# Kernel tuning notes

Measured on AMD Instinct MI355X. Metric: run time of the kernel, lower is better.

## Reference

```python
import jax, jax.numpy as jnp
import numpy as np

# DNC dims: N memory slots, WM word size, R read heads, H controller hidden, D word_vec
N, WM, R, H, D = 256, 64, 4, 512, 512
T, B = 128, 32
EPS = 1e-6
IFACE = R*WM + R + WM + 1 + WM + WM + R + 1 + 1 + 3*R  # DNC interface vector size


def setup_inputs() -> dict:
    key = jax.random.key(0)
    k = jax.random.split(key, 8)
    in_dim = D + R*WM  # controller sees [x_t ; flattened read vectors]
    w = lambda kk, shape: jax.random.normal(kk, shape, jnp.float32) * 0.02
    return {
        "emb_utt": jax.random.normal(k[0], (T, B, D), jnp.float32),
        "Wx": w(k[1], (in_dim, 4*H)),
        "Wh": w(k[2], (H, 4*H)),
        "b_lstm": jnp.zeros((4*H,), jnp.float32),
        "W_pre": w(k[3], (H, D)),
        "b_pre": jnp.zeros((D,), jnp.float32),
        "W_iface": w(k[4], (H, IFACE)),
        "b_iface": jnp.zeros((IFACE,), jnp.float32),
        "W_rout": w(k[5], (R*WM, D)),
    }


def _content(M, keys, beta):
    # M: (B,N,WM); keys: (B,K,WM); beta: (B,K) -> content weighting (B,K,N)
    Mn = M / jnp.maximum(jnp.linalg.norm(M, axis=-1, keepdims=True), EPS)
    kn = keys / jnp.maximum(jnp.linalg.norm(keys, axis=-1, keepdims=True), EPS)
    sim = jnp.einsum('bkw,bnw->bkn', kn, Mn)
    return jax.nn.softmax(beta[..., None] * sim, axis=-1)


def _allocation(u):
    # usage-sort-based allocation weighting (Graves et al. 2016)
    idx = jnp.argsort(u, axis=1)  # ascending usage
    su = jnp.take_along_axis(u, idx, axis=1)
    excl = jnp.concatenate([jnp.ones_like(su[:, :1]), jnp.cumprod(su, axis=1)[:, :-1]], axis=1)
    a_sorted = (1.0 - su) * excl
    bidx = jnp.arange(u.shape[0])[:, None]
    return jnp.zeros_like(u).at[bidx, idx].set(a_sorted)


def reference(emb_utt, Wx, Wh, b_lstm, W_pre, b_pre, W_iface, b_iface, W_rout):
    Bsz = emb_utt.shape[1]
    eye = jnp.eye(N, dtype=emb_utt.dtype)

    def step(carry, x):
        h, c, M, usage, rw, ww, prec, link, rvec = carry
        # ---- controller (LSTM) ----
        xin = jnp.concatenate([x, rvec.reshape(Bsz, -1)], axis=1)
        gates = xin @ Wx + h @ Wh + b_lstm
        i, f, g, o = jnp.split(gates, 4, axis=1)
        c = jax.nn.sigmoid(f) * c + jax.nn.sigmoid(i) * jnp.tanh(g)
        h = jax.nn.sigmoid(o) * jnp.tanh(c)
        # ---- interface ----
        z = h @ W_iface + b_iface
        off = [0]
        def take(n):
            v = z[:, off[0]:off[0]+n]; off[0] += n; return v
        read_keys = take(R*WM).reshape(Bsz, R, WM)
        read_str = 1.0 + jax.nn.softplus(take(R))
        write_key = take(WM)
        write_str = 1.0 + jax.nn.softplus(take(1))
        erase = jax.nn.sigmoid(take(WM))
        write_vec = take(WM)
        free = jax.nn.sigmoid(take(R))
        alloc_g = jax.nn.sigmoid(take(1))
        write_g = jax.nn.sigmoid(take(1))
        modes = jax.nn.softmax(take(3*R).reshape(Bsz, R, 3), axis=-1)
        # ---- memory write ----
        retention = jnp.prod(1.0 - free[:, :, None] * rw, axis=1)   # (B,N)
        usage = (usage + ww - usage * ww) * retention
        alloc = _allocation(usage)
        cw = _content(M, write_key[:, None, :], write_str)[:, 0, :]  # (B,N)
        ww = write_g * (alloc_g * alloc + (1.0 - alloc_g) * cw)
        M = M * (1.0 - ww[:, :, None] * erase[:, None, :]) + ww[:, :, None] * write_vec[:, None, :]
        # temporal link matrix + precedence
        link = (1.0 - ww[:, :, None] - ww[:, None, :]) * link + ww[:, :, None] * prec[:, None, :]
        link = link * (1.0 - eye)
        prec = (1.0 - jnp.sum(ww, axis=1, keepdims=True)) * prec + ww
        # ---- memory read ----
        cr = _content(M, read_keys, read_str)                        # (B,R,N)
        fw = jnp.einsum('bij,brj->bri', link, rw)                    # forward
        bw = jnp.einsum('bji,brj->bri', link, rw)                    # backward
        rw = modes[..., 0:1] * bw + modes[..., 1:2] * cr + modes[..., 2:3] * fw
        rvec = jnp.einsum('brn,bnw->brw', rw, M)
        out = h @ W_pre + b_pre + rvec.reshape(Bsz, -1) @ W_rout
        return (h, c, M, usage, rw, ww, prec, link, rvec), out

    z = lambda *s: jnp.zeros(s, jnp.float32)
    carry0 = (z(Bsz, H), z(Bsz, H), jnp.full((Bsz, N, WM), EPS, jnp.float32),
              z(Bsz, N), z(Bsz, R, N), z(Bsz, N), z(Bsz, N),
              z(Bsz, N, N), z(Bsz, R, WM))
    _, outs = jax.lax.scan(step, carry0, emb_utt)
    return outs  # (T, B, D)
```

## Files before the change

kernel.cpp:

```cpp
#include <hip/hip_runtime.h>
#include <math.h>

#define TN   256
#define TWM  64
#define TR   4
#define TH   512
#define TD   512
#define TT   128
#define TB   32
#define IFACE 471
#define EPSI 1e-6f

#define OFF_H      0
#define OFF_C      32768
#define OFF_M      49152
#define OFF_USAGE  573440
#define OFF_RW     581632
#define OFF_WW     614400
#define OFF_PRECA  622592
#define OFF_LINK   638976
#define OFF_RVEC   2736128
#define OFF_MNORM  2744320
#define OFF_ZP     2752512
#define OFF_PARSE  2998272
#define OFF_CRS    3012608
#define OFF_FW     3045376
#define OFF_BWP    3078144
#define OFF_CNT    3340288
#define TOTAL_STATE 3341696

#define CNT_ZPG(g) (OFF_CNT + (g)*16)
#define CNT_SB(b)  (OFF_CNT + (8+(b))*16)
#define CNT_FA(b)  (OFF_CNT + (40+(b))*16)
#define CNT_GG(g)  (OFF_CNT + (72+(g))*16)

__device__ __forceinline__ float sigm(float x)  { return 1.0f / (1.0f + expf(-x)); }
__device__ __forceinline__ float softpl(float x){ return x > 20.0f ? x : log1pf(expf(x)); }

__device__ __forceinline__ float ldc(const float* p) {
    return __hip_atomic_load(p, __ATOMIC_RELAXED, __HIP_MEMORY_SCOPE_AGENT);
}
__device__ __forceinline__ void stc(float* p, float v) {
    __hip_atomic_store(p, v, __ATOMIC_RELAXED, __HIP_MEMORY_SCOPE_AGENT);
}
__device__ __forceinline__ float4 ldcv4(const float* p) {
    float4 v;
    v.x = ldc(p); v.y = ldc(p + 1); v.z = ldc(p + 2); v.w = ldc(p + 3);
    return v;
}
__device__ __forceinline__ void stcv4(float* p, float4 v) {
    stc(p, v.x); stc(p + 1, v.y); stc(p + 2, v.z); stc(p + 3, v.w);
}

__global__ void k_init(float* ws) {
    int idx = blockIdx.x * 256 + threadIdx.x;
    if (idx >= TOTAL_STATE) return;
    float v = 0.0f;
    if (idx >= OFF_M && idx < OFF_M + TB*TN*TWM) v = EPSI;
    if (idx >= OFF_MNORM && idx < OFF_MNORM + TB*TN) v = 8e-6f;
    ws[idx] = v;
}

__device__ __forceinline__ void out_phase(
    const float* __restrict__ W_pre, const float* __restrict__ b_pre,
    const float* __restrict__ W_rout, const float* __restrict__ ws,
    float* __restrict__ out, float* sm, const int tid, const int B2, const int t)
{
    float* act_s = sm;
    float* red_s = sm + 3072;
    const int q = B2 >> 5, s = (B2 >> 3) & 3, bg = B2 & 7, b0 = bg * 4;
    for (int i = tid; i < 768; i += 512) {
        const int bb = i / 192;
        const int k0 = (i - bb*192) * 4;
        const float* src = (k0 < 512) ? &ws[OFF_H + (t&1)*(TB*TH) + (b0+bb)*TH + k0]
                                      : &ws[OFF_RVEC + (b0+bb)*256 + (k0 - 512)];
        *(float4*)&act_s[bb*768 + k0] = *(const float4*)src;
    }
    __syncthreads();
    const int c0 = q*128 + s*32;
    const int col = tid & 31;
    const int ksb = tid >> 5;
    float a0=0, a1=0, a2=0, a3=0;
    for (int kk = ksb*48; kk < ksb*48 + 48; ++kk) {
        const float w = (kk < 512) ? W_pre[(size_t)kk * 512 + c0 + col]
                                   : W_rout[(size_t)(kk - 512) * 512 + c0 + col];
        a0 += act_s[kk]        * w;
        a1 += act_s[768 + kk]  * w;
        a2 += act_s[1536 + kk] * w;
        a3 += act_s[2304 + kk] * w;
    }
    red_s[(ksb*4 + 0)*32 + col] = a0;
    red_s[(ksb*4 + 1)*32 + col] = a1;
    red_s[(ksb*4 + 2)*32 + col] = a2;
    red_s[(ksb*4 + 3)*32 + col] = a3;
    __syncthreads();
    if (tid < 128) {
        const int cc = tid & 31, bb = tid >> 5;
        float ssum = 0.0f;
        #pragma unroll
        for (int ks2 = 0; ks2 < 16; ++ks2) ssum += red_s[(ks2*4 + bb)*32 + cc];
        ssum += b_pre[c0 + cc];
        out[(size_t)(t - 1) * (TB * TD) + (b0+bb) * TD + c0 + cc] = ssum;
    }
}

__device__ void stepA_fn(const float* __restrict__ b_if, float* __restrict__ ws,
                         const int t, const int b, const int tid, float* sm)
{
    float* z_s      = sm + 0;
    float* rwf_s    = sm + 480;
    float* ww_old_s = sm + 1504;
    float* ww_s     = sm + 1760;
    float* u_s      = sm + 2016;
    float* prec_s   = sm + 2272;
    float* mnorm_s  = sm + 2528;
    float* alloc_s  = sm + 2784;
    float* cw_s     = sm + 3040;
    float* keysp    = sm + 3296;
    float* wkey_s   = sm + 3552;
    float* erase_s  = sm + 3616;
    float* wvec_s   = sm + 3680;
    float* rstr_s   = sm + 3744;
    float* free_s   = sm + 3748;
    float* modesp   = sm + 3752;
    float* knorm_s  = sm + 3764;
    float* sredA_s  = sm + 3772;
    float* sc_s     = sm + 3780;
    float* Pt_s     = sm + 3788;

    const float* wsM = ws + OFF_M + b * (TN * TWM);
    const float* precOld = ws + OFF_PRECA + (t & 1) * (TB * TN) + b * 256;
    float* precNew = ws + OFF_PRECA + ((t + 1) & 1) * (TB * TN) + b * 256;

    if (tid < 256)       { *(float4*)&rwf_s[tid*4] = *(const float4*)&ws[OFF_RW + b*1024 + tid*4]; }
    else if (tid < 320)  { const int i = tid-256; *(float4*)&ww_old_s[i*4] = *(const float4*)&ws[OFF_WW + b*256 + i*4]; }
    else if (tid < 384)  { const int i = tid-320; *(float4*)&u_s[i*4]      = *(const float4*)&ws[OFF_USAGE + b*256 + i*4]; }
    else if (tid < 448)  { const int i = tid-384; *(float4*)&prec_s[i*4]   = *(const float4*)&precOld[i*4]; }
    else                 { const int i = tid-448; *(float4*)&mnorm_s[i*4]  = *(const float4*)&ws[OFF_MNORM + b*256 + i*4]; }
    if (tid < IFACE) {
        float part[16];
        #pragma unroll
        for (int p = 0; p < 16; ++p)
            part[p] = ldc(&ws[OFF_ZP + ((size_t)p*32 + b) * 480 + tid]);
        float zv = b_if[tid];
        #pragma unroll
        for (int p = 0; p < 16; ++p) zv += part[p];
        z_s[tid] = zv;
    }
    __syncthreads();

    if (tid < IFACE) {
        const float v = z_s[tid];
        if (tid < 256)       keysp[(tid >> 6)*64 + (tid & 63)] = v;
        else if (tid < 260)  rstr_s[tid - 256] = 1.0f + softpl(v);
        else if (tid < 324)  wkey_s[tid - 260] = v;
        else if (tid == 324) sc_s[0] = 1.0f + softpl(v);
        else if (tid < 389)  erase_s[tid - 325] = sigm(v);
        else if (tid < 453)  wvec_s[tid - 389] = v;
        else if (tid < 457)  free_s[tid - 453] = sigm(v);
        else if (tid == 457) sc_s[1] = sigm(v);
        else if (tid == 458) sc_s[2] = sigm(v);
    }
    __syncthreads();
    if (tid < 320) {
        const int w5 = tid >> 6, lane = tid & 63;
        const float v = (w5 == 0) ? wkey_s[lane] : keysp[(w5 - 1)*64 + lane];
        float s = v * v;
        #pragma unroll
        for (int m = 1; m <= 32; m <<= 1) s += __shfl_xor(s, m);
        if (lane == 0) knorm_s[w5] = fmaxf(sqrtf(s), EPSI);
    } else if (tid >= 508) {
        const int r = tid - 508;
        const float m0 = z_s[459 + r*3], m1 = z_s[460 + r*3], m2 = z_s[461 + r*3];
        const float mx = fmaxf(m0, fmaxf(m1, m2));
        const float e0 = expf(m0 - mx), e1 = expf(m1 - mx), e2 = expf(m2 - mx);
        const float s = e0 + e1 + e2;
        modesp[r*3+0] = e0 / s; modesp[r*3+1] = e1 / s; modesp[r*3+2] = e2 / s;
    }
    __syncthreads();

    if (tid < 404) {
        float v;
        if (tid < 256)       v = keysp[tid];
        else if (tid < 320)  v = erase_s[tid - 256];
        else if (tid < 384)  v = wvec_s[tid - 320];
        else if (tid < 388)  v = rstr_s[tid - 384];
        else if (tid < 392)  v = knorm_s[tid - 388 + 1];
        else                 v = modesp[tid - 392];
        stc(&ws[OFF_PARSE + b * 448 + tid], v);
    }
    if (tid < 256) {
        float ret = 1.0f;
        #pragma unroll
        for (int r = 0; r < 4; ++r) ret *= 1.0f - free_s[r] * rwf_s[r*256 + tid];
        const float un = (u_s[tid] + ww_old_s[tid] - u_s[tid] * ww_old_s[tid]) * ret;
        u_s[tid] = un;
        ws[OFF_USAGE + b * 256 + tid] = un;
    }
    __syncthreads();

    {
        const int q = tid >> 8, n = tid & 255;
        const float un = u_s[n];
        float p = 1.0f;
        #pragma unroll 8
        for (int m = q * 128; m < q * 128 + 128; ++m) {
            const float um = u_s[m];
            const bool lt = (um < un) || (um == un && m < n);
            p *= lt ? um : 1.0f;
        }
        Pt_s[q * 256 + n] = p;
    }
    __syncthreads();
    if (tid < 256)
        alloc_s[tid] = (1.0f - u_s[tid]) * Pt_s[tid] * Pt_s[256 + tid];
    __syncthreads();

    {
        const int n = tid >> 1, q2 = tid & 1;
        const float* mp = wsM + n * 64 + q2 * 32;
        float s = 0.0f;
        #pragma unroll
        for (int it = 0; it < 8; ++it) {
            float4 mv = *(const float4*)(mp + it * 4);
            float4 kv = *(const float4*)&wkey_s[q2 * 32 + it * 4];
            s += mv.x*kv.x + mv.y*kv.y + mv.z*kv.z + mv.w*kv.w;
        }
        s += __shfl_xor(s, 1);
        if (q2 == 0) cw_s[n] = sc_s[0] * s / (knorm_s[0] * mnorm_s[n]);
    }
    __syncthreads();
    {
        float v = 0.0f, e = 0.0f;
        if (tid < 256) {
            v = cw_s[tid];
            float m = v;
            #pragma unroll
            for (int mm = 1; mm <= 32; mm <<= 1) m = fmaxf(m, __shfl_xor(m, mm));
            if ((tid & 63) == 0) sredA_s[tid >> 6] = m;
        }
        __syncthreads();
        if (tid == 0) sc_s[4] = fmaxf(fmaxf(sredA_s[0], sredA_s[1]), fmaxf(sredA_s[2], sredA_s[3]));
        __syncthreads();
        if (tid < 256) {
            e = expf(v - sc_s[4]);
            float s2 = e;
            #pragma unroll
            for (int mm = 1; mm <= 32; mm <<= 1) s2 += __shfl_xor(s2, mm);
            if ((tid & 63) == 0) sredA_s[tid >> 6] = s2;
        }
        __syncthreads();
        if (tid == 0) sc_s[5] = sredA_s[0] + sredA_s[1] + sredA_s[2] + sredA_s[3];
        __syncthreads();
        if (tid < 256) cw_s[tid] = e / sc_s[5];
    }
    __syncthreads();

    if (tid < 256) {
        const float wwn = sc_s[2] * (sc_s[1] * alloc_s[tid] + (1.0f - sc_s[1]) * cw_s[tid]);
        ww_s[tid] = wwn;
        stc(&ws[OFF_WW + b * 256 + tid], wwn);
    }
    __syncthreads();
    if (tid < 256) {
        float s = ww_s[tid];
        #pragma unroll
        for (int mm = 1; mm <= 32; mm <<= 1) s += __shfl_xor(s, mm);
        if ((tid & 63) == 0) sredA_s[tid >> 6] = s;
    }
    __syncthreads();
    if (tid == 0) sc_s[3] = sredA_s[0] + sredA_s[1] + sredA_s[2] + sredA_s[3];
    __syncthreads();
    if (tid < 256)
        precNew[tid] = (1.0f - sc_s[3]) * prec_s[tid] + ww_s[tid];
}

__device__ void stepB_fn(float* __restrict__ ws, const int t, const int b,
                         const int tid, float* sm)
{
    float* crp     = sm;
    float* rw2_s   = sm + 1024;
    float* Lt2     = sm + 2048;
    float* md      = sm + 4096;
    float* sredA_s = sm + 4112;
    float* sredB_s = sm + 4120;
    float* gmax_s  = sm + 4128;
    float* gsum_s  = sm + 4132;
    const float* wsM = ws + OFF_M + b * (TN * TWM);

    crp[tid]       = ldc(&ws[OFF_CRS + b*1024 + tid]);
    crp[tid + 512] = ldc(&ws[OFF_CRS + b*1024 + tid + 512]);
    if (tid < 12) md[tid] = ldc(&ws[OFF_PARSE + b*448 + 392 + tid]);
    __syncthreads();

    {
        const int rr = tid >> 8, n = tid & 255, wv = tid >> 6, lane = tid & 63;
        float v0 = crp[rr*256 + n], v1 = crp[(rr + 2)*256 + n];
        float m0 = v0, m1 = v1;
        #pragma unroll
        for (int mm = 1; mm <= 32; mm <<= 1) {
            m0 = fmaxf(m0, __shfl_xor(m0, mm));
            m1 = fmaxf(m1, __shfl_xor(m1, mm));
        }
        if (lane == 0) { sredA_s[wv] = m0; sredB_s[wv] = m1; }
        __syncthreads();
        if (tid < 4) {
            const float* base = (tid & 2) ? sredB_s : sredA_s;
            const int off = (tid & 1) * 4;
            gmax_s[tid] = fmaxf(fmaxf(base[off], base[off+1]), fmaxf(base[off+2], base[off+3]));
        }
        __syncthreads();
        const float e0 = expf(v0 - gmax_s[rr]);
        const float e1 = expf(v1 - gmax_s[rr + 2]);
        float s0 = e0, s1 = e1;
        #pragma unroll
        for (int mm = 1; mm <= 32; mm <<= 1) {
            s0 += __shfl_xor(s0, mm); s1 += __shfl_xor(s1, mm);
        }
        if (lane == 0) { sredA_s[wv] = s0; sredB_s[wv] = s1; }
        __syncthreads();
        if (tid < 4) {
            const float* base = (tid & 2) ? sredB_s : sredA_s;
            const int off = (tid & 1) * 4;
            gsum_s[tid] = base[off] + base[off+1] + base[off+2] + base[off+3];
        }
        __syncthreads();
        crp[rr*256 + n]       = e0 / gsum_s[rr];
        crp[(rr + 2)*256 + n] = e1 / gsum_s[rr + 2];
    }
    __syncthreads();

    {
        const int rr = tid >> 8, n = tid & 255;
        #pragma unroll
        for (int p = 0; p < 2; ++p) {
            const int r = rr + 2 * p;
            float part[8];
            #pragma unroll
            for (int c = 0; c < 8; ++c)
                part[c] = ldc(&ws[OFF_BWP + (size_t)(b*8 + c)*1024 + r*256 + n]);
            const float fwv = ldc(&ws[OFF_FW + b*1024 + r*256 + n]);
            float bw = 0.0f;
            #pragma unroll
            for (int c = 0; c < 8; ++c) bw += part[c];
            const float v = md[r*3] * bw + md[r*3+1] * crp[r*256 + n] + md[r*3+2] * fwv;
            rw2_s[r*256 + n] = v;
            ws[OFF_RW + b*1024 + r*256 + n] = v;
        }
    }
    __syncthreads();

    {
        const int g8 = tid >> 6, w = tid & 63;
        float p0=0, p1=0, p2=0, p3=0;
        const float* mb = wsM + (size_t)(g8 * 32) * 64 + w;
        for (int gg = 0; gg < 4; ++gg) {
            float mv[8];
            #pragma unroll
            for (int j = 0; j < 8; ++j) mv[j] = ldc(mb + (gg*8 + j) * 64);
            #pragma unroll
            for (int j = 0; j < 8; ++j) {
                const int n = g8*32 + gg*8 + j;
                p0 += rw2_s[n]       * mv[j];
                p1 += rw2_s[256 + n] * mv[j];
                p2 += rw2_s[512 + n] * mv[j];
                p3 += rw2_s[768 + n] * mv[j];
            }
        }
        Lt2[(g8*4 + 0)*64 + w] = p0;
        Lt2[(g8*4 + 1)*64 + w] = p1;
        Lt2[(g8*4 + 2)*64 + w] = p2;
        Lt2[(g8*4 + 3)*64 + w] = p3;
    }
    __syncthreads();
    if (tid < 256) {
        const int r = tid >> 6, w = tid & 63;
        float s = 0.0f;
        #pragma unroll
        for (int g = 0; g < 8; ++g) s += Lt2[(g*4 + r)*64 + w];
        ws[OFF_RVEC + b * 256 + tid] = s;
    }
}

__global__ __launch_bounds__(512) void k_all(
    const float* __restrict__ emb, const float* __restrict__ Wx,
    const float* __restrict__ Wh,  const float* __restrict__ b_lstm,
    const float* __restrict__ W_pre, const float* __restrict__ b_pre,
    const float* __restrict__ W_rout,
    const float* __restrict__ W_if, const float* __restrict__ b_if,
    float* __restrict__ ws, float* __restrict__ out, int t)
{
    __shared__ __align__(16) float sm[16384];
    __shared__ int myBatch;
    __shared__ int isTail;
    const int tid = threadIdx.x;
    const int blk = blockIdx.x;

    if (blk >= 128) {
        if (t > 0) {
            const int raw2 = blk - 128;
            const int B2 = (((raw2 >> 2) & 3) << 5) | ((raw2 & 3) << 3) | (raw2 >> 4);
            out_phase(W_pre, b_pre, W_rout, ws, out, sm, tid, B2, t);
        }
    } else if (t < TT) {
        const int ublk = ((blk & 7) << 4) | (blk >> 3);
        const int u0  = ublk * 4;
        {
            const int cg  = tid & 3;
            const int bg  = (tid >> 2) & 7;
            const int ks  = tid >> 5;
            const int col0 = cg * 512 + u0;
            const float* hbuf = ws + OFF_H + (t & 1) * (TB * TH);

            float acc[4][4] = {};

            for (int tile = 0; tile < 5; ++tile) {
                const int T0 = tile * 256;
                {
                    const int b = tid & 31, kf4 = tid >> 5;
                    #pragma unroll
                    for (int i = 0; i < 4; ++i) {
                        const int kf = kf4 * 4 + i;
                        const int kl = kf * 4;
                        const int k  = T0 + kl;
                        const float* src;
                        if (k < 512)      src = emb + (size_t)t * (TB*TD) + b * TD + k;
                        else if (k < 768) src = ws + OFF_RVEC + b * 256 + (k - 512);
                        else              src = hbuf + b * TH + (k - 768);
                        float4 v = *(const float4*)src;
                        sm[(kl+0)*32 + b] = v.x;
                        sm[(kl+1)*32 + b] = v.y;
                        sm[(kl+2)*32 + b] = v.z;
                        sm[(kl+3)*32 + b] = v.w;
                    }
                }
                __syncthreads();
                {
                    const int k0 = T0 + ks * 16;
                    const float* wp = (k0 < 768 ? Wx + (size_t)k0 * 2048
                                                : Wh + (size_t)(k0 - 768) * 2048) + col0;
                    const float* ap = &sm[(ks * 16) * 32 + bg * 4];
                    #pragma unroll 8
                    for (int kk = 0; kk < 16; ++kk) {
                        float4 wv = *(const float4*)wp; wp += 2048;
                        float4 av = *(const float4*)ap; ap += 32;
                        acc[0][0] += wv.x*av.x; acc[0][1] += wv.x*av.y; acc[0][2] += wv.x*av.z; acc[0][3] += wv.x*av.w;
                        acc[1][0] += wv.y*av.x; acc[1][1] += wv.y*av.y; acc[1][2] += wv.y*av.z; acc[1][3] += wv.y*av.w;
                        acc[2][0] += wv.z*av.x; acc[2][1] += wv.z*av.y; acc[2][2] += wv.z*av.z; acc[2][3] += wv.z*av.w;
                        acc[3][0] += wv.w*av.x; acc[3][1] += wv.w*av.y; acc[3][2] += wv.w*av.z; acc[3][3] += wv.w*av.w;
                    }
                }
                __syncthreads();
            }

            {
                const int rbase = 8192 + ks * 512 + (cg * 8 + bg) * 16;
                *(float4*)&sm[rbase + 0]  = make_float4(acc[0][0], acc[0][1], acc[0][2], acc[0][3]);
                *(float4*)&sm[rbase + 4]  = make_float4(acc[1][0], acc[1][1], acc[1][2], acc[1][3]);
                *(float4*)&sm[rbase + 8]  = make_float4(acc[2][0], acc[2][1], acc[2][2], acc[2][3]);
                *(float4*)&sm[rbase + 12] = make_float4(acc[3][0], acc[3][1], acc[3][2], acc[3][3]);
            }
            __syncthreads();
            {
                const int o = tid;
                float s = 0.0f;
                #pragma unroll
                for (int kq = 0; kq < 16; ++kq) s += sm[8192 + kq * 512 + o];
                const int ocg = o >> 7, obg = (o >> 4) & 7, odu = (o >> 2) & 3, obb = o & 3;
                s += b_lstm[ocg * 512 + u0 + odu];
                sm[(ocg * 4 + odu) * 32 + (obg * 4 + obb)] = s;
            }
            __syncthreads();
            if (tid < 128) {
                const int du = tid >> 5, b = tid & 31;
                const float ig = sm[(0  + du) * 32 + b];
                const float fg = sm[(4  + du) * 32 + b];
                const float gg = sm[(8  + du) * 32 + b];
                const float og = sm[(12 + du) * 32 + b];
                const int ci = b * TH + u0 + du;
                const float cold = ws[OFF_C + ci];
                const float cn = sigm(fg) * cold + sigm(ig) * tanhf(gg);
                const float hn = sigm(og) * tanhf(cn);
                ws[OFF_C + ci] = cn;
                stc(&ws[OFF_H + ((t + 1) & 1) * (TB * TH) + ci], hn);
            }
        }
        asm volatile("s_waitcnt vmcnt(0)" ::: "memory");
        __syncthreads();
        if (tid == 0)
            __hip_atomic_fetch_add((unsigned*)(ws + CNT_GG(ublk >> 3)), 1u,
                                   __ATOMIC_RELAXED, __HIP_MEMORY_SCOPE_AGENT);

        const int bgz = blk >> 4;
        const int q = (blk >> 2) & 3, s = blk & 3;
        const int b0 = bgz * 4;
        if (tid == 0) {
            const unsigned* gg = (const unsigned*)(ws + CNT_GG(q*4 + s));
            while (__hip_atomic_load(gg, __ATOMIC_RELAXED, __HIP_MEMORY_SCOPE_AGENT) < 8u * (unsigned)(t + 1))
                __builtin_amdgcn_s_sleep(2);
        }
        __syncthreads();
        {
            float* h1_s = sm;
            if (tid < 128) {
                const int bb = tid >> 5, kk = tid & 31;
                h1_s[bb*32 + kk] = ldc(&ws[OFF_H + ((t+1)&1)*(TB*TH) + (b0+bb)*TH + q*128 + s*32 + kk]);
            }
            __syncthreads();
            if (tid < IFACE) {
                const int col = tid;
                float a0=0, a1=0, a2=0, a3=0;
                const float* wb = W_if + (size_t)(q*128 + s*32) * IFACE + col;
                #pragma unroll 8
                for (int kk = 0; kk < 32; ++kk) {
                    const float w = *wb; wb += IFACE;
                    a0 += h1_s[kk]      * w;
                    a1 += h1_s[32+kk]   * w;
                    a2 += h1_s[64+kk]   * w;
                    a3 += h1_s[96+kk]   * w;
                }
                const size_t base = OFF_ZP + ((size_t)(q*4+s)*32 + b0) * 480 + col;
                stc(&ws[base],        a0);
                stc(&ws[base + 480],  a1);
                stc(&ws[base + 960],  a2);
                stc(&ws[base + 1440], a3);
            }
        }
        asm volatile("s_waitcnt vmcnt(0)" ::: "memory");
        __syncthreads();
        if (tid == 0) {
            unsigned* cnt = (unsigned*)(ws + CNT_ZPG(bgz));
            const unsigned old = __hip_atomic_fetch_add(cnt, 1u, __ATOMIC_RELAXED, __HIP_MEMORY_SCOPE_AGENT);
            const unsigned base = 16u * (unsigned)t;
            int mb = -1;
            if (old >= base + 12u) {
                mb = b0 + (int)(old - (base + 12u));
                while (__hip_atomic_load(cnt, __ATOMIC_RELAXED, __HIP_MEMORY_SCOPE_AGENT) < base + 16u)
                    __builtin_amdgcn_s_sleep(2);
            }
            myBatch = mb;
        }
        __syncthreads();
        if (myBatch >= 0) {
            stepA_fn(b_if, ws, t, myBatch, tid, sm);
            asm volatile("s_waitcnt vmcnt(0)" ::: "memory");
            __syncthreads();
            if (tid == 0)
                __hip_atomic_store((unsigned*)(ws + CNT_FA(myBatch)), (unsigned)(t + 1),
                                   __ATOMIC_RELAXED, __HIP_MEMORY_SCOPE_AGENT);
        }
    }

    if (t >= TT) return;

    const int b = blk >> 3;
    const int c = blk & 7;
    if (tid == 0) {
        const unsigned* fa = (const unsigned*)(ws + CNT_FA(b));
        while (__hip_atomic_load(fa, __ATOMIC_RELAXED, __HIP_MEMORY_SCOPE_AGENT) < (unsigned)(t + 1))
            __builtin_amdgcn_s_sleep(2);
    }
    __syncthreads();
    asm volatile("" ::: "memory");

    {
        float* ww_s   = sm;
        float* prec_s = sm + 256;
        float* rw_s   = sm + 512;
        float* pk_s   = sm + 1536;
        float* Lt     = sm + 2048;
        const float* precOld = ws + OFF_PRECA + (t & 1) * (TB * TN) + b * 256;

        if (tid < 64)        { *(float4*)&ww_s[tid*4] = ldcv4(&ws[OFF_WW + b*256 + tid*4]); }
        else if (tid < 128)  { const int i = tid-64;  *(float4*)&prec_s[i*4] = *(const float4*)&precOld[i*4]; }
        else if (tid < 384)  { const int i = tid-128; *(float4*)&rw_s[i*4]   = *(const float4*)&ws[OFF_RW + b*1024 + i*4]; }
        else if (tid < 496)  { const int i = tid-384; *(float4*)&pk_s[i*4]   = ldcv4(&ws[OFF_PARSE + b*448 + i*4]); }
        __syncthreads();

        {
            const int ric = tid >> 4, c4 = (tid & 15) * 4;
            const int gi  = c * 32 + ric;
            float* mp = ws + OFF_M + b * (TN*TWM) + gi * 64 + c4;
            float4 m = *(const float4*)mp;
            const float wwi = ww_s[gi];
            float4 er = *(const float4*)&pk_s[256 + c4];
            float4 wv = *(const float4*)&pk_s[320 + c4];
            m.x = m.x * (1.0f - wwi * er.x) + wwi * wv.x;
            m.y = m.y * (1.0f - wwi * er.y) + wwi * wv.y;
            m.z = m.z * (1.0f - wwi * er.z) + wwi * wv.z;
            m.w = m.w * (1.0f - wwi * er.w) + wwi * wv.w;
            stcv4(mp, m);
            float sn = m.x*m.x + m.y*m.y + m.z*m.z + m.w*m.w;
            float d0 = m.x*pk_s[c4]     + m.y*pk_s[c4+1]     + m.z*pk_s[c4+2]     + m.w*pk_s[c4+3];
            float d1 = m.x*pk_s[64+c4]  + m.y*pk_s[64+c4+1]  + m.z*pk_s[64+c4+2]  + m.w*pk_s[64+c4+3];
            float d2 = m.x*pk_s[128+c4] + m.y*pk_s[128+c4+1] + m.z*pk_s[128+c4+2] + m.w*pk_s[128+c4+3];
            float d3 = m.x*pk_s[192+c4] + m.y*pk_s[192+c4+1] + m.z*pk_s[192+c4+2] + m.w*pk_s[192+c4+3];
            #pragma unroll
            for (int mm = 1; mm <= 8; mm <<= 1) {
                sn += __shfl_xor(sn, mm);
                d0 += __shfl_xor(d0, mm); d1 += __shfl_xor(d1, mm);
                d2 += __shfl_xor(d2, mm); d3 += __shfl_xor(d3, mm);
            }
            if ((tid & 15) == 0) {
                const float mn = fmaxf(sqrtf(sn), EPSI);
                ws[OFF_MNORM + b*256 + gi] = mn;
                const float inv = 1.0f / mn;
                stc(&ws[OFF_CRS + b*1024 + 0*256 + gi], pk_s[384+0] * d0 * inv / pk_s[388+0]);
                stc(&ws[OFF_CRS + b*1024 + 1*256 + gi], pk_s[384+1] * d1 * inv / pk_s[388+1]);
                stc(&ws[OFF_CRS + b*1024 + 2*256 + gi], pk_s[384+2] * d2 * inv / pk_s[388+2]);
                stc(&ws[OFF_CRS + b*1024 + 3*256 + gi], pk_s[384+3] * d3 * inv / pk_s[388+3]);
            }
        }

        {
            const int j = tid & 255, p = tid >> 8;
            const float wwj = ww_s[j], pj = prec_s[j];
            #pragma unroll 4
            for (int it = 0; it < 16; ++it) {
                const int ric = it * 2 + p;
                const int gi  = c * 32 + ric;
                float* lp = ws + OFF_LINK + (size_t)b * (TN*TN) + (size_t)gi * 256 + j;
                const float wwi = ww_s[gi];
                float v = (1.0f - wwi - wwj) * (*lp) + wwi * pj;
                if (j == gi) v = 0.0f;
                *lp = v;
                Lt[ric * 257 + j] = v;
            }
        }
        __syncthreads();

        {
            const int ric = tid >> 4, g = tid & 15;
            const int gi = c * 32 + ric;
            float f0=0, f1=0, f2=0, f3=0;
            #pragma unroll 4
            for (int jj = 0; jj < 16; ++jj) {
                const int j = g * 16 + jj;
                const float v = Lt[ric * 257 + j];
                f0 += v * rw_s[j]; f1 += v * rw_s[256+j];
                f2 += v * rw_s[512+j]; f3 += v * rw_s[768+j];
            }
            #pragma unroll
            for (int mm = 1; mm <= 8; mm <<= 1) {
                f0 += __shfl_xor(f0, mm); f1 += __shfl_xor(f1, mm);
                f2 += __shfl_xor(f2, mm); f3 += __shfl_xor(f3, mm);
            }
            if (g == 0) {
                stc(&ws[OFF_FW + b*1024 + gi],       f0);
                stc(&ws[OFF_FW + b*1024 + 256 + gi], f1);
                stc(&ws[OFF_FW + b*1024 + 512 + gi], f2);
                stc(&ws[OFF_FW + b*1024 + 768 + gi], f3);
            }
        }

        {
            const int j = tid & 255, p = tid >> 8;
            float b0=0, b1=0, b2=0, b3=0;
            #pragma unroll 4
            for (int it = 0; it < 16; ++it) {
                const int ric = p * 16 + it;
                const int gi  = c * 32 + ric;
                const float v = Lt[ric * 257 + j];
                b0 += v * rw_s[gi]; b1 += v * rw_s[256+gi];
                b2 += v * rw_s[512+gi]; b3 += v * rw_s[768+gi];
            }
            __syncthreads();
            if (p == 1) { Lt[j] = b0; Lt[256+j] = b1; Lt[512+j] = b2; Lt[768+j] = b3; }
            __syncthreads();
            if (p == 0) {
                stc(&ws[OFF_BWP + (size_t)blk*1024 + j],       b0 + Lt[j]);
                stc(&ws[OFF_BWP + (size_t)blk*1024 + 256 + j], b1 + Lt[256+j]);
                stc(&ws[OFF_BWP + (size_t)blk*1024 + 512 + j], b2 + Lt[512+j]);
                stc(&ws[OFF_BWP + (size_t)blk*1024 + 768 + j], b3 + Lt[768+j]);
            }
        }
    }

    asm volatile("s_waitcnt vmcnt(0)" ::: "memory");
    __syncthreads();
    if (tid == 0) {
        unsigned* cnt = (unsigned*)(ws + CNT_SB(b));
        const unsigned old = __hip_atomic_fetch_add(cnt, 1u, __ATOMIC_RELAXED, __HIP_MEMORY_SCOPE_AGENT);
        isTail = (old == 8u * (unsigned)t + 7u) ? 1 : 0;
    }
    __syncthreads();
    if (!isTail) return;
    stepB_fn(ws, t, b, tid, sm);
}

extern "C" void kernel_launch(void* const* d_in, const int* in_sizes, int n_in,
                              void* d_out, int out_size, void* d_ws, size_t ws_size,
                              hipStream_t stream) {
    const float* emb    = (const float*)d_in[0];
    const float* Wx     = (const float*)d_in[1];
    const float* Wh     = (const float*)d_in[2];
    const float* b_lstm = (const float*)d_in[3];
    const float* W_pre  = (const float*)d_in[4];
    const float* b_pre  = (const float*)d_in[5];
    const float* W_if   = (const float*)d_in[6];
    const float* b_if   = (const float*)d_in[7];
    const float* W_rout = (const float*)d_in[8];
    float* out = (float*)d_out;
    float* ws  = (float*)d_ws;

    k_init<<<(TOTAL_STATE + 255) / 256, 256, 0, stream>>>(ws);
    for (int t = 0; t < TT; ++t) {
        k_all<<<256, 512, 0, stream>>>(emb, Wx, Wh, b_lstm, W_pre, b_pre, W_rout,
                                       W_if, b_if, ws, out, t);
    }
    k_all<<<256, 512, 0, stream>>>(emb, Wx, Wh, b_lstm, W_pre, b_pre, W_rout,
                                   W_if, b_if, ws, out, TT);
}
```

Baseline: 7.253 ms.

## Fuse all timesteps into one persistent cooperative kernel with counter-based sync

Replaces the 129 per-timestep kernel launches with a single cooperative persistent kernel that loops over time internally. Cross-block dependencies are enforced with atomic counters and spin-waits, including a new all-batch read-vector counter. The read vector is double-buffered, and the Wx tile order is changed so the emb and h tiles are processed before waiting on the previous read vectors. Cross-block state now goes through agent-scope atomic loads and stores, which adds per-element overhead and risks stalls if spin-wait dependencies are mis-ordered.

```diff
diff --git a/kernel.cpp b/kernel.cpp
--- a/kernel.cpp
+++ b/kernel.cpp
@@ -27,12 +27,14 @@
 #define OFF_FW     3045376
 #define OFF_BWP    3078144
 #define OFF_CNT    3340288
-#define TOTAL_STATE 3341696
+#define OFF_RVECB  3341824
+#define TOTAL_STATE 3350016
 
 #define CNT_ZPG(g) (OFF_CNT + (g)*16)
 #define CNT_SB(b)  (OFF_CNT + (8+(b))*16)
 #define CNT_FA(b)  (OFF_CNT + (40+(b))*16)
 #define CNT_GG(g)  (OFF_CNT + (72+(g))*16)
+#define CNT_RVALL  (OFF_CNT + 88*16)
 
 __device__ __forceinline__ float sigm(float x)  { return 1.0f / (1.0f + expf(-x)); }
 __device__ __forceinline__ float softpl(float x){ return x > 20.0f ? x : log1pf(expf(x)); }
@@ -50,6 +52,9 @@
 }
 __device__ __forceinline__ void stcv4(float* p, float4 v) {
     stc(p, v.x); stc(p + 1, v.y); stc(p + 2, v.z); stc(p + 3, v.w);
+}
+__device__ __forceinline__ unsigned ldcu(const unsigned* p) {
+    return __hip_atomic_load(p, __ATOMIC_RELAXED, __HIP_MEMORY_SCOPE_AGENT);
 }
 
 __global__ void k_init(float* ws) {
@@ -61,9 +66,10 @@
     ws[idx] = v;
 }
 
-__device__ __forceinline__ void out_phase(
+__device__ void out_phase_p(
     const float* __restrict__ W_pre, const float* __restrict__ b_pre,
-    const float* __restrict__ W_rout, const float* __restrict__ ws,
+    const float* __restrict__ W_rout,
+    const float* __restrict__ hsrc, const float* __restrict__ rsrc,
     float* __restrict__ out, float* sm, const int tid, const int B2, const int t)
 {
     float* act_s = sm;
@@ -72,9 +78,9 @@
     for (int i = tid; i < 768; i += 512) {
         const int bb = i / 192;
         const int k0 = (i - bb*192) * 4;
-        const float* src = (k0 < 512) ? &ws[OFF_H + (t&1)*(TB*TH) + (b0+bb)*TH + k0]
-                                      : &ws[OFF_RVEC + (b0+bb)*256 + (k0 - 512)];
-        *(float4*)&act_s[bb*768 + k0] = *(const float4*)src;
+        const float* src = (k0 < 512) ? &hsrc[(b0+bb)*TH + k0]
+                                      : &rsrc[(b0+bb)*256 + (k0 - 512)];
+        *(float4*)&act_s[bb*768 + k0] = ldcv4(src);
     }
     __syncthreads();
     const int c0 = q*128 + s*32;
@@ -102,6 +108,7 @@
         ssum += b_pre[c0 + cc];
         out[(size_t)(t - 1) * (TB * TD) + (b0+bb) * TD + c0 + cc] = ssum;
     }
+    __syncthreads();
 }
 
 __device__ void stepA_fn(const float* __restrict__ b_if, float* __restrict__ ws,
@@ -132,11 +139,11 @@
     const float* precOld = ws + OFF_PRECA + (t & 1) * (TB * TN) + b * 256;
     float* precNew = ws + OFF_PRECA + ((t + 1) & 1) * (TB * TN) + b * 256;
 
-    if (tid < 256)       { *(float4*)&rwf_s[tid*4] = *(const float4*)&ws[OFF_RW + b*1024 + tid*4]; }
-    else if (tid < 320)  { const int i = tid-256; *(float4*)&ww_old_s[i*4] = *(const float4*)&ws[OFF_WW + b*256 + i*4]; }
-    else if (tid < 384)  { const int i = tid-320; *(float4*)&u_s[i*4]      = *(const float4*)&ws[OFF_USAGE + b*256 + i*4]; }
-    else if (tid < 448)  { const int i = tid-384; *(float4*)&prec_s[i*4]   = *(const float4*)&precOld[i*4]; }
-    else                 { const int i = tid-448; *(float4*)&mnorm_s[i*4]  = *(const float4*)&ws[OFF_MNORM + b*256 + i*4]; }
+    if (tid < 256)       { *(float4*)&rwf_s[tid*4] = ldcv4(&ws[OFF_RW + b*1024 + tid*4]); }
+    else if (tid < 320)  { const int i = tid-256; *(float4*)&ww_old_s[i*4] = ldcv4(&ws[OFF_WW + b*256 + i*4]); }
+    else if (tid < 384)  { const int i = tid-320; *(float4*)&u_s[i*4]      = ldcv4(&ws[OFF_USAGE + b*256 + i*4]); }
+    else if (tid < 448)  { const int i = tid-384; *(float4*)&prec_s[i*4]   = ldcv4(&precOld[i*4]); }
+    else                 { const int i = tid-448; *(float4*)&mnorm_s[i*4]  = ldcv4(&ws[OFF_MNORM + b*256 + i*4]); }
     if (tid < IFACE) {
         float part[16];
         #pragma unroll
@@ -195,7 +202,7 @@
         for (int r = 0; r < 4; ++r) ret *= 1.0f - free_s[r] * rwf_s[r*256 + tid];
         const float un = (u_s[tid] + ww_old_s[tid] - u_s[tid] * ww_old_s[tid]) * ret;
         u_s[tid] = un;
-        ws[OFF_USAGE + b * 256 + tid] = un;
+        stc(&ws[OFF_USAGE + b * 256 + tid], un);
     }
     __syncthreads();
 
@@ -222,7 +229,7 @@
         float s = 0.0f;
         #pragma unroll
         for (int it = 0; it < 8; ++it) {
-            float4 mv = *(const float4*)(mp + it * 4);
+            float4 mv = ldcv4(mp + it * 4);
             float4 kv = *(const float4*)&wkey_s[q2 * 32 + it * 4];
             s += mv.x*kv.x + mv.y*kv.y + mv.z*kv.z + mv.w*kv.w;
         }
@@ -272,11 +279,11 @@
     if (tid == 0) sc_s[3] = sredA_s[0] + sredA_s[1] + sredA_s[2] + sredA_s[3];
     __syncthreads();
     if (tid < 256)
-        precNew[tid] = (1.0f - sc_s[3]) * prec_s[tid] + ww_s[tid];
-}
-
-__device__ void stepB_fn(float* __restrict__ ws, const int t, const int b,
-                         const int tid, float* sm)
+        stc(&precNew[tid], (1.0f - sc_s[3]) * prec_s[tid] + ww_s[tid]);
+}
+
+__device__ void stepB_fn(float* __restrict__ ws, float* __restrict__ rvnew,
+                         const int t, const int b, const int tid, float* sm)
 {
     float* crp     = sm;
     float* rw2_s   = sm + 1024;
@@ -345,7 +352,7 @@
             for (int c = 0; c < 8; ++c) bw += part[c];
             const float v = md[r*3] * bw + md[r*3+1] * crp[r*256 + n] + md[r*3+2] * fwv;
             rw2_s[r*256 + n] = v;
-            ws[OFF_RW + b*1024 + r*256 + n] = v;
+            stc(&ws[OFF_RW + b*1024 + r*256 + n], v);
         }
     }
     __syncthreads();
@@ -378,17 +385,17 @@
         float s = 0.0f;
         #pragma unroll
         for (int g = 0; g < 8; ++g) s += Lt2[(g*4 + r)*64 + w];
-        ws[OFF_RVEC + b * 256 + tid] = s;
-    }
-}
-
-__global__ __launch_bounds__(512) void k_all(
+        stc(&rvnew[b * 256 + tid], s);
+    }
+}
+
+__global__ __launch_bounds__(512) void k_dnc(
     const float* __restrict__ emb, const float* __restrict__ Wx,
     const float* __restrict__ Wh,  const float* __restrict__ b_lstm,
     const float* __restrict__ W_pre, const float* __restrict__ b_pre,
     const float* __restrict__ W_rout,
     const float* __restrict__ W_if, const float* __restrict__ b_if,
-    float* __restrict__ ws, float* __restrict__ out, int t)
+    float* __restrict__ ws, float* __restrict__ out)
 {
     __shared__ __align__(16) float sm[16384];
     __shared__ int myBatch;
@@ -396,296 +403,329 @@
     const int tid = threadIdx.x;
     const int blk = blockIdx.x;
 
-    if (blk >= 128) {
-        if (t > 0) {
-            const int raw2 = blk - 128;
-            const int B2 = (((raw2 >> 2) & 3) << 5) | ((raw2 & 3) << 3) | (raw2 >> 4);
-            out_phase(W_pre, b_pre, W_rout, ws, out, sm, tid, B2, t);
-        }
-    } else if (t < TT) {
-        const int ublk = ((blk & 7) << 4) | (blk >> 3);
-        const int u0  = ublk * 4;
-        {
-            const int cg  = tid & 3;
-            const int bg  = (tid >> 2) & 7;
-            const int ks  = tid >> 5;
-            const int col0 = cg * 512 + u0;
-            const float* hbuf = ws + OFF_H + (t & 1) * (TB * TH);
-
-            float acc[4][4] = {};
-
-            for (int tile = 0; tile < 5; ++tile) {
-                const int T0 = tile * 256;
+    for (int t = 0; t < TT; ++t) {
+        float* rvnew = ws + ((t & 1) ? OFF_RVECB : OFF_RVEC);
+        const float* rvold = ws + (((t + 1) & 1) ? OFF_RVECB : OFF_RVEC);
+
+        if (blk < 128) {
+            const int ublk = ((blk & 7) << 4) | (blk >> 3);
+            const int u0  = ublk * 4;
+            {
+                const int cg  = tid & 3;
+                const int bg  = (tid >> 2) & 7;
+                const int ks  = tid >> 5;
+                const int col0 = cg * 512 + u0;
+                const float* hbuf = ws + OFF_H + (t & 1) * (TB * TH);
+
+                float acc[4][4] = {};
+
+                #pragma unroll
+                for (int ii = 0; ii < 5; ++ii) {
+                    const int tile = (ii < 2) ? ii : (ii == 4 ? 2 : ii + 1);
+                    const int T0 = tile * 256;
+                    if (tile == 2) {
+                        if (tid == 0) {
+                            const unsigned* p = (const unsigned*)(ws + CNT_RVALL);
+                            while (ldcu(p) < 32u * (unsigned)t) __builtin_amdgcn_s_sleep(2);
+                        }
+                        __syncthreads();
+                    }
+                    {
+                        const int b = tid & 31, kf4 = tid >> 5;
+                        #pragma unroll
+                        for (int i = 0; i < 4; ++i) {
+                            const int kl = (kf4 * 4 + i) * 4;
+                            const int k  = T0 + kl;
+                            float4 v;
+                            if (tile < 2)       v = *(const float4*)(emb + (size_t)t * (TB*TD) + b * TD + k);
+                            else if (tile == 2) v = ldcv4(rvold + b * 256 + (k - 512));
+                            else                v = ldcv4(hbuf + b * TH + (k - 768));
+                            sm[(kl+0)*32 + b] = v.x;
+                            sm[(kl+1)*32 + b] = v.y;
+                            sm[(kl+2)*32 + b] = v.z;
+                            sm[(kl+3)*32 + b] = v.w;
+                        }
+                    }
+                    __syncthreads();
+                    {
+                        const int k0 = T0 + ks * 16;
+                        const float* wp = (k0 < 768 ? Wx + (size_t)k0 * 2048
+                                                    : Wh + (size_t)(k0 - 768) * 2048) + col0;
+                        const float* ap = &sm[(ks * 16) * 32 + bg * 4];
+                        #pragma unroll 8
+                        for (int kk = 0; kk < 16; ++kk) {
+                            float4 wv = *(const float4*)wp; wp += 2048;
+                            float4 av = *(const float4*)ap; ap += 32;
+                            acc[0][0] += wv.x*av.x; acc[0][1] += wv.x*av.y; acc[0][2] += wv.x*av.z; acc[0][3] += wv.x*av.w;
+                            acc[1][0] += wv.y*av.x; acc[1][1] += wv.y*av.y; acc[1][2] += wv.y*av.z; acc[1][3] += wv.y*av.w;
+                            acc[2][0] += wv.z*av.x; acc[2][1] += wv.z*av.y; acc[2][2] += wv.z*av.z; acc[2][3] += wv.z*av.w;
+                            acc[3][0] += wv.w*av.x; acc[3][1] += wv.w*av.y; acc[3][2] += wv.w*av.z; acc[3][3] += wv.w*av.w;
+                        }
+                    }
+                    __syncthreads();
+                }
+
                 {
-                    const int b = tid & 31, kf4 = tid >> 5;
-                    #pragma unroll
-                    for (int i = 0; i < 4; ++i) {
-                        const int kf = kf4 * 4 + i;
-                        const int kl = kf * 4;
-                        const int k  = T0 + kl;
-                        const float* src;
-                        if (k < 512)      src = emb + (size_t)t * (TB*TD) + b * TD + k;
-                        else if (k < 768) src = ws + OFF_RVEC + b * 256 + (k - 512);
-                        else              src = hbuf + b * TH + (k - 768);
-                        float4 v = *(const float4*)src;
-                        sm[(kl+0)*32 + b] = v.x;
-                        sm[(kl+1)*32 + b] = v.y;
-                        sm[(kl+2)*32 + b] = v.z;
-                        sm[(kl+3)*32 + b] = v.w;
-                    }
+                    const int rbase = 8192 + ks * 512 + (cg * 8 + bg) * 16;
+                    *(float4*)&sm[rbase + 0]  = make_float4(acc[0][0], acc[0][1], acc[0][2], acc[0][3]);
+                    *(float4*)&sm[rbase + 4]  = make_float4(acc[1][0], acc[1][1], acc[1][2], acc[1][3]);
+                    *(float4*)&sm[rbase + 8]  = make_float4(acc[2][0], acc[2][1], acc[2][2], acc[2][3]);
+                    *(float4*)&sm[rbase + 12] = make_float4(acc[3][0], acc[3][1], acc[3][2], acc[3][3]);
                 }
                 __syncthreads();
                 {
-                    const int k0 = T0 + ks * 16;
-                    const float* wp = (k0 < 768 ? Wx + (size_t)k0 * 2048
-                                                : Wh + (size_t)(k0 - 768) * 2048) + col0;
-                    const float* ap = &sm[(ks * 16) * 32 + bg * 4];
-                    #pragma unroll 8
-                    for (int kk = 0; kk < 16; ++kk) {
-                        float4 wv = *(const float4*)wp; wp += 2048;
-                        float4 av = *(const float4*)ap; ap += 32;
-                        acc[0][0] += wv.x*av.x; acc[0][1] += wv.x*av.y; acc[0][2] += wv.x*av.z; acc[0][3] += wv.x*av.w;
-                        acc[1][0] += wv.y*av.x; acc[1][1] += wv.y*av.y; acc[1][2] += wv.y*av.z; acc[1][3] += wv.y*av.w;
-                        acc[2][0] += wv.z*av.x; acc[2][1] += wv.z*av.y; acc[2][2] += wv.z*av.z; acc[2][3] += wv.z*av.w;
-                        acc[3][0] += wv.w*av.x; acc[3][1] += wv.w*av.y; acc[3][2] += wv.w*av.z; acc[3][3] += wv.w*av.w;
-                    }
+                    const int o = tid;
+                    float s = 0.0f;
+                    #pragma unroll
+                    for (int kq = 0; kq < 16; ++kq) s += sm[8192 + kq * 512 + o];
+                    const int ocg = o >> 7, obg = (o >> 4) & 7, odu = (o >> 2) & 3, obb = o & 3;
+                    s += b_lstm[ocg * 512 + u0 + odu];
+                    sm[(ocg * 4 + odu) * 32 + (obg * 4 + obb)] = s;
                 }
                 __syncthreads();
-            }
-
-            {
-                const int rbase = 8192 + ks * 512 + (cg * 8 + bg) * 16;
-                *(float4*)&sm[rbase + 0]  = make_float4(acc[0][0], acc[0][1], acc[0][2], acc[0][3]);
-                *(float4*)&sm[rbase + 4]  = make_float4(acc[1][0], acc[1][1], acc[1][2], acc[1][3]);
-                *(float4*)&sm[rbase + 8]  = make_float4(acc[2][0], acc[2][1], acc[2][2], acc[2][3]);
-                *(float4*)&sm[rbase + 12] = make_float4(acc[3][0], acc[3][1], acc[3][2], acc[3][3]);
-            }
-            __syncthreads();
-            {
-                const int o = tid;
-                float s = 0.0f;
-                #pragma unroll
-                for (int kq = 0; kq < 16; ++kq) s += sm[8192 + kq * 512 + o];
-                const int ocg = o >> 7, obg = (o >> 4) & 7, odu = (o >> 2) & 3, obb = o & 3;
-                s += b_lstm[ocg * 512 + u0 + odu];
-                sm[(ocg * 4 + odu) * 32 + (obg * 4 + obb)] = s;
-            }
-            __syncthreads();
-            if (tid < 128) {
-                const int du = tid >> 5, b = tid & 31;
-                const float ig = sm[(0  + du) * 32 + b];
-                const float fg = sm[(4  + du) * 32 + b];
-                const float gg = sm[(8  + du) * 32 + b];
-                const float og = sm[(12 + du) * 32 + b];
-                const int ci = b * TH + u0 + du;
-                const float cold = ws[OFF_C + ci];
-                const float cn = sigm(fg) * cold + sigm(ig) * tanhf(gg);
-                const float hn = sigm(og) * tanhf(cn);
-                ws[OFF_C + ci] = cn;
-                stc(&ws[OFF_H + ((t + 1) & 1) * (TB * TH) + ci], hn);
-            }
-        }
-        asm volatile("s_waitcnt vmcnt(0)" ::: "memory");
-        __syncthreads();
-        if (tid == 0)
-            __hip_atomic_fetch_add((unsigned*)(ws + CNT_GG(ublk >> 3)), 1u,
-                                   __ATOMIC_RELAXED, __HIP_MEMORY_SCOPE_AGENT);
-
-        const int bgz = blk >> 4;
-        const int q = (blk >> 2) & 3, s = blk & 3;
-        const int b0 = bgz * 4;
-        if (tid == 0) {
-            const unsigned* gg = (const unsigned*)(ws + CNT_GG(q*4 + s));
-            while (__hip_atomic_load(gg, __ATOMIC_RELAXED, __HIP_MEMORY_SCOPE_AGENT) < 8u * (unsigned)(t + 1))
-                __builtin_amdgcn_s_sleep(2);
-        }
-        __syncthreads();
-        {
-            float* h1_s = sm;
-            if (tid < 128) {
-                const int bb = tid >> 5, kk = tid & 31;
-                h1_s[bb*32 + kk] = ldc(&ws[OFF_H + ((t+1)&1)*(TB*TH) + (b0+bb)*TH + q*128 + s*32 + kk]);
-            }
-            __syncthreads();
-            if (tid < IFACE) {
-                const int col = tid;
-                float a0=0, a1=0, a2=0, a3=0;
-                const float* wb = W_if + (size_t)(q*128 + s*32) * IFACE + col;
-                #pragma unroll 8
-                for (int kk = 0; kk < 32; ++kk) {
-                    const float w = *wb; wb += IFACE;
-                    a0 += h1_s[kk]      * w;
-                    a1 += h1_s[32+kk]   * w;
-                    a2 += h1_s[64+kk]   * w;
-                    a3 += h1_s[96+kk]   * w;
-                }
-                const size_t base = OFF_ZP + ((size_t)(q*4+s)*32 + b0) * 480 + col;
-                stc(&ws[base],        a0);
-                stc(&ws[base + 480],  a1);
-                stc(&ws[base + 960],  a2);
-                stc(&ws[base + 1440], a3);
-            }
-        }
-        asm volatile("s_waitcnt vmcnt(0)" ::: "memory");
-        __syncthreads();
-        if (tid == 0) {
-            unsigned* cnt = (unsigned*)(ws + CNT_ZPG(bgz));
-            const unsigned old = __hip_atomic_fetch_add(cnt, 1u, __ATOMIC_RELAXED, __HIP_MEMORY_SCOPE_AGENT);
-            const unsigned base = 16u * (unsigned)t;
-            int mb = -1;
-            if (old >= base + 12u) {
-                mb = b0 + (int)(old - (base + 12u));
-                while (__hip_atomic_load(cnt, __ATOMIC_RELAXED, __HIP_MEMORY_SCOPE_AGENT) < base + 16u)
-                    __builtin_amdgcn_s_sleep(2);
-            }
-            myBatch = mb;
-        }
-        __syncthreads();
-        if (myBatch >= 0) {
-            stepA_fn(b_if, ws, t, myBatch, tid, sm);
+                if (tid < 128) {
+                    const int du = tid >> 5, b = tid & 31;
+                    const float ig = sm[(0  + du) * 32 + b];
+                    const float fg = sm[(4  + du) * 32 + b];
+                    const float gg = sm[(8  + du) * 32 + b];
+                    const float og = sm[(12 + du) * 32 + b];
+                    const int ci = b * TH + u0 + du;
+                    const float cold = ws[OFF_C + ci];
+                    const float cn = sigm(fg) * cold + sigm(ig) * tanhf(gg);
+                    const float hn = sigm(og) * tanhf(cn);
+                    ws[OFF_C + ci] = cn;
+                    stc(&ws[OFF_H + ((t + 1) & 1) * (TB * TH) + ci], hn);
+                }
+            }
             asm volatile("s_waitcnt vmcnt(0)" ::: "memory");
             __syncthreads();
             if (tid == 0)
-                __hip_atomic_store((unsigned*)(ws + CNT_FA(myBatch)), (unsigned)(t + 1),
-                                   __ATOMIC_RELAXED, __HIP_MEMORY_SCOPE_AGENT);
-        }
-    }
-
-    if (t >= TT) return;
-
-    const int b = blk >> 3;
-    const int c = blk & 7;
-    if (tid == 0) {
-        const unsigned* fa = (const unsigned*)(ws + CNT_FA(b));
-        while (__hip_atomic_load(fa, __ATOMIC_RELAXED, __HIP_MEMORY_SCOPE_AGENT) < (unsigned)(t + 1))
-            __builtin_amdgcn_s_sleep(2);
-    }
-    __syncthreads();
-    asm volatile("" ::: "memory");
-
-    {
-        float* ww_s   = sm;
-        float* prec_s = sm + 256;
-        float* rw_s   = sm + 512;
-        float* pk_s   = sm + 1536;
-        float* Lt     = sm + 2048;
-        const float* precOld = ws + OFF_PRECA + (t & 1) * (TB * TN) + b * 256;
-
-        if (tid < 64)        { *(float4*)&ww_s[tid*4] = ldcv4(&ws[OFF_WW + b*256 + tid*4]); }
-        else if (tid < 128)  { const int i = tid-64;  *(float4*)&prec_s[i*4] = *(const float4*)&precOld[i*4]; }
-        else if (tid < 384)  { const int i = tid-128; *(float4*)&rw_s[i*4]   = *(const float4*)&ws[OFF_RW + b*1024 + i*4]; }
-        else if (tid < 496)  { const int i = tid-384; *(float4*)&pk_s[i*4]   = ldcv4(&ws[OFF_PARSE + b*448 + i*4]); }
+                __hip_atomic_fetch_add((unsigned*)(ws + CNT_GG(ublk >> 3)), 1u,
+                                       __ATOMIC_RELAXED, __HIP_MEMORY_SCOPE_AGENT);
+
+            const int bgz = blk >> 4;
+            const int q = (blk >> 2) & 3, s = blk & 3;
+            const int b0 = bgz * 4;
+            if (tid == 0) {
+                const unsigned* gg = (const unsigned*)(ws + CNT_GG(q*4 + s));
+                while (ldcu(gg) < 8u * (unsigned)(t + 1)) __builtin_amdgcn_s_sleep(2);
+            }
+            __syncthreads();
+            {
+                float* h1_s = sm;
+                if (tid < 128) {
+                    const int bb = tid >> 5, kk = tid & 31;
+                    h1_s[bb*32 + kk] = ldc(&ws[OFF_H + ((t+1)&1)*(TB*TH) + (b0+bb)*TH + q*128 + s*32 + kk]);
+                }
+                __syncthreads();
+                if (tid < IFACE) {
+                    const int col = tid;
+                    float a0=0, a1=0, a2=0, a3=0;
+                    const float* wb = W_if + (size_t)(q*128 + s*32) * IFACE + col;
+                    #pragma unroll 8
+                    for (int kk = 0; kk < 32; ++kk) {
+                        const float w = *wb; wb += IFACE;
+                        a0 += h1_s[kk]      * w;
+                        a1 += h1_s[32+kk]   * w;
+                        a2 += h1_s[64+kk]   * w;
+                        a3 += h1_s[96+kk]   * w;
+                    }
+                    const size_t base = OFF_ZP + ((size_t)(q*4+s)*32 + b0) * 480 + col;
+                    stc(&ws[base],        a0);
+                    stc(&ws[base + 480],  a1);
+                    stc(&ws[base + 960],  a2);
+                    stc(&ws[base + 1440], a3);
+                }
+            }
+            asm volatile("s_waitcnt vmcnt(0)" ::: "memory");
+            __syncthreads();
+            if (tid == 0) {
+                unsigned* cnt = (unsigned*)(ws + CNT_ZPG(bgz));
+                const unsigned old = __hip_atomic_fetch_add(cnt, 1u, __ATOMIC_RELAXED, __HIP_MEMORY_SCOPE_AGENT);
+                const unsigned base = 16u * (unsigned)t;
+                int mb = -1;
+                if (old >= base + 12u) {
+                    mb = b0 + (int)(old - (base + 12u));
+                    while (ldcu(cnt) < base + 16u) __builtin_amdgcn_s_sleep(2);
+                }
+                myBatch = mb;
+            }
+            __syncthreads();
+            if (myBatch >= 0) {
+                stepA_fn(b_if, ws, t, myBatch, tid, sm);
+                asm volatile("s_waitcnt vmcnt(0)" ::: "memory");
+                __syncthreads();
+                if (tid == 0)
+                    __hip_atomic_store((unsigned*)(ws + CNT_FA(myBatch)), (unsigned)(t + 1),
+                                       __ATOMIC_RELAXED, __HIP_MEMORY_SCOPE_AGENT);
+            }
+            __syncthreads();
+        } else {
+            if (t > 0) {
+                if (tid == 0) {
+                    const unsigned* p = (const unsigned*)(ws + CNT_RVALL);
+                    while (ldcu(p) < 32u * (unsigned)t) __builtin_amdgcn_s_sleep(2);
+                }
+                __syncthreads();
+                const int raw2 = blk - 128;
+                const int B2 = (((raw2 >> 2) & 3) << 5) | ((raw2 & 3) << 3) | (raw2 >> 4);
+                out_phase_p(W_pre, b_pre, W_rout, ws + OFF_H + (t & 1) * (TB * TH),
+                            rvold, out, sm, tid, B2, t);
+            }
+        }
+
+        const int b = blk >> 3;
+        const int c = blk & 7;
+        if (tid == 0) {
+            const unsigned* fa = (const unsigned*)(ws + CNT_FA(b));
+            while (ldcu(fa) < (unsigned)(t + 1)) __builtin_amdgcn_s_sleep(2);
+        }
         __syncthreads();
 
         {
-            const int ric = tid >> 4, c4 = (tid & 15) * 4;
-            const int gi  = c * 32 + ric;
-            float* mp = ws + OFF_M + b * (TN*TWM) + gi * 64 + c4;
-            float4 m = *(const float4*)mp;
-            const float wwi = ww_s[gi];
-            float4 er = *(const float4*)&pk_s[256 + c4];
-            float4 wv = *(const float4*)&pk_s[320 + c4];
-            m.x = m.x * (1.0f - wwi * er.x) + wwi * wv.x;
-            m.y = m.y * (1.0f - wwi * er.y) + wwi * wv.y;
-            m.z = m.z * (1.0f - wwi * er.z) + wwi * wv.z;
-            m.w = m.w * (1.0f - wwi * er.w) + wwi * wv.w;
-            stcv4(mp, m);
-            float sn = m.x*m.x + m.y*m.y + m.z*m.z + m.w*m.w;
-            float d0 = m.x*pk_s[c4]     + m.y*pk_s[c4+1]     + m.z*pk_s[c4+2]     + m.w*pk_s[c4+3];
-            float d1 = m.x*pk_s[64+c4]  + m.y*pk_s[64+c4+1]  + m.z*pk_s[64+c4+2]  + m.w*pk_s[64+c4+3];
-            float d2 = m.x*pk_s[128+c4] + m.y*pk_s[128+c4+1] + m.z*pk_s[128+c4+2] + m.w*pk_s[128+c4+3];
-            float d3 = m.x*pk_s[192+c4] + m.y*pk_s[192+c4+1] + m.z*pk_s[192+c4+2] + m.w*pk_s[192+c4+3];
-            #pragma unroll
-            for (int mm = 1; mm <= 8; mm <<= 1) {
-                sn += __shfl_xor(sn, mm);
-                d0 += __shfl_xor(d0, mm); d1 += __shfl_xor(d1, mm);
-                d2 += __shfl_xor(d2, mm); d3 += __shfl_xor(d3, mm);
-            }
-            if ((tid & 15) == 0) {
-                const float mn = fmaxf(sqrtf(sn), EPSI);
-                ws[OFF_MNORM + b*256 + gi] = mn;
-                const float inv = 1.0f / mn;
-                stc(&ws[OFF_CRS + b*1024 + 0*256 + gi], pk_s[384+0] * d0 * inv / pk_s[388+0]);
-                stc(&ws[OFF_CRS + b*1024 + 1*256 + gi], pk_s[384+1] * d1 * inv / pk_s[388+1]);
-                stc(&ws[OFF_CRS + b*1024 + 2*256 + gi], pk_s[384+2] * d2 * inv / pk_s[388+2]);
-                stc(&ws[OFF_CRS + b*1024 + 3*256 + gi], pk_s[384+3] * d3 * inv / pk_s[388+3]);
-            }
-        }
-
-        {
-            const int j = tid & 255, p = tid >> 8;
-            const float wwj = ww_s[j], pj = prec_s[j];
-            #pragma unroll 4
-            for (int it = 0; it < 16; ++it) {
-                const int ric = it * 2 + p;
+            float* ww_s   = sm;
+            float* prec_s = sm + 256;
+            float* rw_s   = sm + 512;
+            float* pk_s   = sm + 1536;
+            float* Lt     = sm + 2048;
+            const float* precOld = ws + OFF_PRECA + (t & 1) * (TB * TN) + b * 256;
+
+            if (tid < 64)        { *(float4*)&ww_s[tid*4] = ldcv4(&ws[OFF_WW + b*256 + tid*4]); }
+            else if (tid < 128)  { const int i = tid-64;  *(float4*)&prec_s[i*4] = ldcv4(&precOld[i*4]); }
+            else if (tid < 384)  { const int i = tid-128; *(float4*)&rw_s[i*4]   = ldcv4(&ws[OFF_RW + b*1024 + i*4]); }
+            else if (tid < 496)  { const int i = tid-384; *(float4*)&pk_s[i*4]   = ldcv4(&ws[OFF_PARSE + b*448 + i*4]); }
+            __syncthreads();
+
+            {
+                const int ric = tid >> 4, c4 = (tid & 15) * 4;
                 const int gi  = c * 32 + ric;
-                float* lp = ws + OFF_LINK + (size_t)b * (TN*TN) + (size_t)gi * 256 + j;
+                float* mp = ws + OFF_M + b * (TN*TWM) + gi * 64 + c4;
+                float4 m = ldcv4(mp);
                 const float wwi = ww_s[gi];
-                float v = (1.0f - wwi - wwj) * (*lp) + wwi * pj;
-                if (j == gi) v = 0.0f;
-                *lp = v;
-                Lt[ric * 257 + j] = v;
-            }
-        }
-        __syncthreads();
-
-        {
-            const int ric = tid >> 4, g = tid & 15;
-            const int gi = c * 32 + ric;
-            float f0=0, f1=0, f2=0, f3=0;
-            #pragma unroll 4
-            for (int jj = 0; jj < 16; ++jj) {
-                const int j = g * 16 + jj;
-                const float v = Lt[ric * 257 + j];
-                f0 += v * rw_s[j]; f1 += v * rw_s[256+j];
-                f2 += v * rw_s[512+j]; f3 += v * rw_s[768+j];
-            }
-            #pragma unroll
-            for (int mm = 1; mm <= 8; mm <<= 1) {
-                f0 += __shfl_xor(f0, mm); f1 += __shfl_xor(f1, mm);
-                f2 += __shfl_xor(f2, mm); f3 += __shfl_xor(f3, mm);
-            }
-            if (g == 0) {
-                stc(&ws[OFF_FW + b*1024 + gi],       f0);
-                stc(&ws[OFF_FW + b*1024 + 256 + gi], f1);
-                stc(&ws[OFF_FW + b*1024 + 512 + gi], f2);
-                stc(&ws[OFF_FW + b*1024 + 768 + gi], f3);
-            }
-        }
-
-        {
-            const int j = tid & 255, p = tid >> 8;
-            float b0=0, b1=0, b2=0, b3=0;
-            #pragma unroll 4
-            for (int it = 0; it < 16; ++it) {
-                const int ric = p * 16 + it;
-                const int gi  = c * 32 + ric;
-                const float v = Lt[ric * 257 + j];
-                b0 += v * rw_s[gi]; b1 += v * rw_s[256+gi];
-                b2 += v * rw_s[512+gi]; b3 += v * rw_s[768+gi];
+                float4 er = *(const float4*)&pk_s[256 + c4];
+                float4 wv = *(const float4*)&pk_s[320 + c4];
+                m.x = m.x * (1.0f - wwi * er.x) + wwi * wv.x;
+                m.y = m.y * (1.0f - wwi * er.y) + wwi * wv.y;
+                m.z = m.z * (1.0f - wwi * er.z) + wwi * wv.z;
+                m.w = m.w * (1.0f - wwi * er.w) + wwi * wv.w;
+                stcv4(mp, m);
+                float sn = m.x*m.x + m.y*m.y + m.z*m.z + m.w*m.w;
+                float d0 = m.x*pk_s[c4]     + m.y*pk_s[c4+1]     + m.z*pk_s[c4+2]     + m.w*pk_s[c4+3];
+                float d1 = m.x*pk_s[64+c4]  + m.y*pk_s[64+c4+1]  + m.z*pk_s[64+c4+2]  + m.w*pk_s[64+c4+3];
+                float d2 = m.x*pk_s[128+c4] + m.y*pk_s[128+c4+1] + m.z*pk_s[128+c4+2] + m.w*pk_s[128+c4+3];
+                float d3 = m.x*pk_s[192+c4] + m.y*pk_s[192+c4+1] + m.z*pk_s[192+c4+2] + m.w*pk_s[192+c4+3];
+                #pragma unroll
+                for (int mm = 1; mm <= 8; mm <<= 1) {
+                    sn += __shfl_xor(sn, mm);
+                    d0 += __shfl_xor(d0, mm); d1 += __shfl_xor(d1, mm);
+                    d2 += __shfl_xor(d2, mm); d3 += __shfl_xor(d3, mm);
+                }
+                if ((tid & 15) == 0) {
+                    const float mn = fmaxf(sqrtf(sn), EPSI);
+                    stc(&ws[OFF_MNORM + b*256 + gi], mn);
+                    const float inv = 1.0f / mn;
+                    stc(&ws[OFF_CRS + b*1024 + 0*256 + gi], pk_s[384+0] * d0 * inv / pk_s[388+0]);
+                    stc(&ws[OFF_CRS + b*1024 + 1*256 + gi], pk_s[384+1] * d1 * inv / pk_s[388+1]);
+                    stc(&ws[OFF_CRS + b*1024 + 2*256 + gi], pk_s[384+2] * d2 * inv / pk_s[388+2]);
+                    stc(&ws[OFF_CRS + b*1024 + 3*256 + gi], pk_s[384+3] * d3 * inv / pk_s[388+3]);
+                }
+            }
+
+            {
+                const int j = tid & 255, p = tid >> 8;
+                const float wwj = ww_s[j], pj = prec_s[j];
+                #pragma unroll 4
+                for (int it = 0; it < 16; ++it) {
+                    const int ric = it * 2 + p;
+                    const int gi  = c * 32 + ric;
+                    float* lp = ws + OFF_LINK + (size_t)b * (TN*TN) + (size_t)gi * 256 + j;
+                    const float wwi = ww_s[gi];
+                    float v = (1.0f - wwi - wwj) * (*lp) + wwi * pj;
+                    if (j == gi) v = 0.0f;
+                    *lp = v;
+                    Lt[ric * 257 + j] = v;
+                }
             }
             __syncthreads();
-            if (p == 1) { Lt[j] = b0; Lt[256+j] = b1; Lt[512+j] = b2; Lt[768+j] = b3; }
+
+            {
+                const int ric = tid >> 4, g = tid & 15;
+                const int gi = c * 32 + ric;
+                float f0=0, f1=0, f2=0, f3=0;
+                #pragma unroll 4
+                for (int jj = 0; jj < 16; ++jj) {
+                    const int j = g * 16 + jj;
+                    const float v = Lt[ric * 257 + j];
+                    f0 += v * rw_s[j]; f1 += v * rw_s[256+j];
+                    f2 += v * rw_s[512+j]; f3 += v * rw_s[768+j];
+                }
+                #pragma unroll
+                for (int mm = 1; mm <= 8; mm <<= 1) {
+                    f0 += __shfl_xor(f0, mm); f1 += __shfl_xor(f1, mm);
+                    f2 += __shfl_xor(f2, mm); f3 += __shfl_xor(f3, mm);
+                }
+                if (g == 0) {
+                    stc(&ws[OFF_FW + b*1024 + gi],       f0);
+                    stc(&ws[OFF_FW + b*1024 + 256 + gi], f1);
+                    stc(&ws[OFF_FW + b*1024 + 512 + gi], f2);
+                    stc(&ws[OFF_FW + b*1024 + 768 + gi], f3);
+                }
+            }
+
+            {
+                const int j = tid & 255, p = tid >> 8;
+                float b0=0, b1=0, b2=0, b3=0;
+                #pragma unroll 4
+                for (int it = 0; it < 16; ++it) {
+                    const int ric = p * 16 + it;
+                    const int gi  = c * 32 + ric;
+                    const float v = Lt[ric * 257 + j];
+                    b0 += v * rw_s[gi]; b1 += v * rw_s[256+gi];
+                    b2 += v * rw_s[512+gi]; b3 += v * rw_s[768+gi];
+                }
+                __syncthreads();
+                if (p == 1) { Lt[j] = b0; Lt[256+j] = b1; Lt[512+j] = b2; Lt[768+j] = b3; }
+                __syncthreads();
+                if (p == 0) {
+                    stc(&ws[OFF_BWP + (size_t)blk*1024 + j],       b0 + Lt[j]);
+                    stc(&ws[OFF_BWP + (size_t)blk*1024 + 256 + j], b1 + Lt[256+j]);
+                    stc(&ws[OFF_BWP + (size_t)blk*1024 + 512 + j], b2 + Lt[512+j]);
+                    stc(&ws[OFF_BWP + (size_t)blk*1024 + 768 + j], b3 + Lt[768+j]);
+                }
+            }
+        }
+
+        asm volatile("s_waitcnt vmcnt(0)" ::: "memory");
+        __syncthreads();
+        if (tid == 0) {
+            unsigned* cnt = (unsigned*)(ws + CNT_SB(b));
+            const unsigned old = __hip_atomic_fetch_add(cnt, 1u, __ATOMIC_RELAXED, __HIP_MEMORY_SCOPE_AGENT);
+            isTail = (old == 8u * (unsigned)t + 7u) ? 1 : 0;
+        }
+        __syncthreads();
+        if (isTail) {
+            stepB_fn(ws, rvnew, t, b, tid, sm);
+            asm volatile("s_waitcnt vmcnt(0)" ::: "memory");
             __syncthreads();
-            if (p == 0) {
-                stc(&ws[OFF_BWP + (size_t)blk*1024 + j],       b0 + Lt[j]);
-                stc(&ws[OFF_BWP + (size_t)blk*1024 + 256 + j], b1 + Lt[256+j]);
-                stc(&ws[OFF_BWP + (size_t)blk*1024 + 512 + j], b2 + Lt[512+j]);
-                stc(&ws[OFF_BWP + (size_t)blk*1024 + 768 + j], b3 + Lt[768+j]);
-            }
-        }
-    }
-
-    asm volatile("s_waitcnt vmcnt(0)" ::: "memory");
-    __syncthreads();
-    if (tid == 0) {
-        unsigned* cnt = (unsigned*)(ws + CNT_SB(b));
-        const unsigned old = __hip_atomic_fetch_add(cnt, 1u, __ATOMIC_RELAXED, __HIP_MEMORY_SCOPE_AGENT);
-        isTail = (old == 8u * (unsigned)t + 7u) ? 1 : 0;
-    }
-    __syncthreads();
-    if (!isTail) return;
-    stepB_fn(ws, t, b, tid, sm);
+            if (tid == 0)
+                __hip_atomic_fetch_add((unsigned*)(ws + CNT_RVALL), 1u,
+                                       __ATOMIC_RELAXED, __HIP_MEMORY_SCOPE_AGENT);
+        }
+        __syncthreads();
+    }
+
+    if (blk >= 128) {
+        if (tid == 0) {
+            const unsigned* p = (const unsigned*)(ws + CNT_RVALL);
+            while (ldcu(p) < 32u * (unsigned)TT) __builtin_amdgcn_s_sleep(2);
+        }
+        __syncthreads();
+        const int raw2 = blk - 128;
+        const int B2 = (((raw2 >> 2) & 3) << 5) | ((raw2 & 3) << 3) | (raw2 >> 4);
+        const float* rvlast = ws + (((TT + 1) & 1) ? OFF_RVECB : OFF_RVEC);
+        out_phase_p(W_pre, b_pre, W_rout, ws + OFF_H + (TT & 1) * (TB * TH),
+                    rvlast, out, sm, tid, B2, TT);
+    }
 }
 
 extern "C" void kernel_launch(void* const* d_in, const int* in_sizes, int n_in,
@@ -704,10 +744,9 @@
     float* ws  = (float*)d_ws;
 
     k_init<<<(TOTAL_STATE + 255) / 256, 256, 0, stream>>>(ws);
-    for (int t = 0; t < TT; ++t) {
-        k_all<<<256, 512, 0, stream>>>(emb, Wx, Wh, b_lstm, W_pre, b_pre, W_rout,
-                                       W_if, b_if, ws, out, t);
-    }
-    k_all<<<256, 512, 0, stream>>>(emb, Wx, Wh, b_lstm, W_pre, b_pre, W_rout,
-                                   W_if, b_if, ws, out, TT);
-}
+
+    void* args[] = { (void*)&emb, (void*)&Wx, (void*)&Wh, (void*)&b_lstm,
+                     (void*)&W_pre, (void*)&b_pre, (void*)&W_rout,
+                     (void*)&W_if, (void*)&b_if, (void*)&ws, (void*)&out };
+    hipLaunchCooperativeKernel(k_dnc, dim3(256), dim3(512), args, 0, stream);
+}
```

Result: slower. 10.93 ms (+50.6%).
